# Kernel tuning notes

Hardware: AMD Instinct MI355X
Metric: run time of the kernel (lower is better)

Reference implementation:

```python
import jax, jax.numpy as jnp
import numpy as np
from jax import lax

N, L, D = 8, 2048, 512
KS = [3, 5]
DECAY = 0.2


def setup_inputs() -> dict:
    key = jax.random.key(0)
    k1, k2, k3, k4, k5 = jax.random.split(key, 5)
    return {
        "qa_embed_data": jax.random.normal(k1, (N, L, D), dtype=jnp.float32),
        "conv_w3": jax.random.normal(k2, (D, 1, KS[0]), dtype=jnp.float32) * (1.0 / KS[0]),
        "conv_w5": jax.random.normal(k3, (D, 1, KS[1]), dtype=jnp.float32) * (1.0 / KS[1]),
        "fusion_w": jax.random.normal(k4, (D, 2 * D), dtype=jnp.float32) * 0.02,
        "fusion_b": jax.random.normal(k5, (D,), dtype=jnp.float32) * 0.02,
    }


def causal_depthwise_conv(x, w, k):
    # x: [N, L, C], w: [C, 1, k] (depthwise, groups=C). Left-pad by k-1 (causal).
    xc = jnp.transpose(x, (0, 2, 1))  # [N, C, L]
    y = lax.conv_general_dilated(
        xc, w, window_strides=(1,), padding=[(k - 1, 0)],
        feature_group_count=x.shape[-1],
        dimension_numbers=("NCH", "OIH", "NCH"))
    return jnp.transpose(y, (0, 2, 1))  # [N, L, C]


def squash(v):
    norm = jnp.linalg.norm(v, axis=-1, keepdims=True)
    scale = norm ** 2 / (1.0 + norm ** 2)
    return scale * v / (norm + 1e-9)


def dynamic_routing(u, num_iterations):
    # u: [N, L, M, C]
    n, l, m, _ = u.shape
    logits = jnp.zeros((n, l, m), dtype=u.dtype)
    v = None
    for i in range(num_iterations):
        c = jax.nn.softmax(logits, axis=-1)
        s = jnp.einsum("nlm,nlmc->nlc", c, u)
        v = squash(s)
        if i < num_iterations - 1:
            logits = logits + jnp.einsum("nlmc,nlc->nlm", u, v)
    return v


def time_attention(x):
    # x: [N, L, C]; causal attention with exp(-decay*dist) bias -> add -decay*dist in log space
    l = x.shape[1]
    sim = jnp.einsum("nlc,nmc->nlm", x, x)  # [N, L, L]
    idx = jnp.arange(l)
    dist = (idx[:, None] - idx[None, :]).astype(x.dtype)  # query - key
    mask = dist >= 0  # lower-triangular causal mask
    ws = jnp.where(mask[None], sim - DECAY * dist[None], -jnp.inf)
    attn = jax.nn.softmax(ws, axis=-1)
    return jnp.einsum("nlm,nmc->nlc", attn, x)


def reference(qa_embed_data, conv_w3, conv_w5, fusion_w, fusion_b):
    trend3 = causal_depthwise_conv(qa_embed_data, conv_w3, KS[0])
    trend5 = causal_depthwise_conv(qa_embed_data, conv_w5, KS[1])
    seasonal = jnp.stack([qa_embed_data - trend3, qa_embed_data - trend5], axis=2)  # [N,L,2,C]
    trend = jnp.stack([trend3, trend5], axis=2)  # [N,L,2,C]
    seasonal_f = time_attention(dynamic_routing(seasonal, 3))
    trend_f = time_attention(dynamic_routing(trend, 3))
    cat = jnp.concatenate([seasonal_f, trend_f], axis=-1)  # [N,L,2C]
    return cat @ fusion_w.T + fusion_b
```

## Files before the change

### kernel.cpp

```cpp
#include <hip/hip_runtime.h>


typedef short     bf16x8 __attribute__((ext_vector_type(8)));
typedef float     f32x4  __attribute__((ext_vector_type(4)));
typedef unsigned short u16;
typedef u16       u16x8  __attribute__((ext_vector_type(8)));

#define NBATCH 8
#define LSEQ   2048
#define DCH    512
#define DPAD   520
#define DECAYF 0.2f
#define WTILES 4

typedef const __attribute__((address_space(1))) unsigned char* gas_t;
typedef __attribute__((address_space(3))) unsigned char* las_t;
__device__ __forceinline__ void dma16(const void* g, void* l) {
    __builtin_amdgcn_global_load_lds((gas_t)g, (las_t)l, 16, 0, 0);
}

__device__ __forceinline__ u16 f2bf(float f) {
    unsigned int u = __float_as_uint(f);
    u += 0x7fffu + ((u >> 16) & 1u);
    return (u16)(u >> 16);
}

__device__ __forceinline__ void wave_sum6(float& a, float& b, float& c,
                                          float& d, float& e, float& f) {
#pragma unroll
    for (int m = 1; m < 64; m <<= 1) {
        float ta = __shfl_xor(a, m, 64);
        float tb = __shfl_xor(b, m, 64);
        float tc = __shfl_xor(c, m, 64);
        float td = __shfl_xor(d, m, 64);
        float te = __shfl_xor(e, m, 64);
        float tf = __shfl_xor(f, m, 64);
        a += ta; b += tb; c += tc; d += td; e += te; f += tf;
    }
}

__global__ __launch_bounds__(256) void conv_route(
    const float* __restrict__ x, const float* __restrict__ w3, const float* __restrict__ w5,
    u16* __restrict__ vs, u16* __restrict__ vt)
{
    const int wid  = threadIdx.x >> 6;
    const int lane = threadIdx.x & 63;
    const int p = blockIdx.x * 4 + wid;
    const int n = p >> 11, l = p & (LSEQ - 1);
    const int c0 = lane * 8;

    float xm[5][8];
#pragma unroll
    for (int j = 0; j < 5; ++j) {
        int ll = l - j;
        if (ll >= 0) {
            const float4* sp = (const float4*)(x + ((size_t)(n*LSEQ + ll))*DCH + c0);
            float4 a = sp[0], b = sp[1];
            xm[j][0]=a.x; xm[j][1]=a.y; xm[j][2]=a.z; xm[j][3]=a.w;
            xm[j][4]=b.x; xm[j][5]=b.y; xm[j][6]=b.z; xm[j][7]=b.w;
        } else {
#pragma unroll
            for (int i = 0; i < 8; ++i) xm[j][i] = 0.f;
        }
    }
    float f3[24], f5[40];
#pragma unroll
    for (int k = 0; k < 6; ++k)  ((float4*)f3)[k] = ((const float4*)(w3 + (size_t)c0*3))[k];
#pragma unroll
    for (int k = 0; k < 10; ++k) ((float4*)f5)[k] = ((const float4*)(w5 + (size_t)c0*5))[k];

    float t3[8], t5[8], a0[8], a1[8];
#pragma unroll
    for (int i = 0; i < 8; ++i) {
        t3[i] = f3[i*3+0]*xm[2][i] + f3[i*3+1]*xm[1][i] + f3[i*3+2]*xm[0][i];
        t5[i] = f5[i*5+0]*xm[4][i] + f5[i*5+1]*xm[3][i] + f5[i*5+2]*xm[2][i]
              + f5[i*5+3]*xm[1][i] + f5[i*5+4]*xm[0][i];
        a0[i] = xm[0][i] - t3[i];
        a1[i] = xm[0][i] - t5[i];
    }

    float A1=0.f, B1=0.f, C1=0.f, A2=0.f, B2=0.f, C2=0.f;
#pragma unroll
    for (int i = 0; i < 8; ++i) {
        A1 += a0[i]*a0[i]; B1 += a0[i]*a1[i]; C1 += a1[i]*a1[i];
        A2 += t3[i]*t3[i]; B2 += t3[i]*t5[i]; C2 += t5[i]*t5[i];
    }
    wave_sum6(A1, B1, C1, A2, B2, C2);

    float ba0=0.f, ba1=0.f, bb0=0.f, bb1=0.f;
    float ca0=0.5f, ca1=0.5f, sca=0.f, cb0=0.5f, cb1=0.5f, scb=0.f;
#pragma unroll
    for (int it = 0; it < 3; ++it) {
        float mxa = fmaxf(ba0, ba1), mxb = fmaxf(bb0, bb1);
        float ea0 = __expf(ba0-mxa), ea1 = __expf(ba1-mxa);
        float eb0 = __expf(bb0-mxb), eb1 = __expf(bb1-mxb);
        float ia = 1.f/(ea0+ea1), ib = 1.f/(eb0+eb1);
        ca0 = ea0*ia; ca1 = ea1*ia; cb0 = eb0*ib; cb1 = eb1*ib;
        float na = ca0*ca0*A1 + 2.f*ca0*ca1*B1 + ca1*ca1*C1;
        float nb = cb0*cb0*A2 + 2.f*cb0*cb1*B2 + cb1*cb1*C2;
        sca = na / ((1.f + na) * (sqrtf(na) + 1e-9f));
        scb = nb / ((1.f + nb) * (sqrtf(nb) + 1e-9f));
        if (it < 2) {
            ba0 += sca*(ca0*A1 + ca1*B1);
            ba1 += sca*(ca0*B1 + ca1*C1);
            bb0 += scb*(cb0*A2 + cb1*B2);
            bb1 += scb*(cb0*B2 + cb1*C2);
        }
    }
    u16x8 pa, pb;
#pragma unroll
    for (int i = 0; i < 8; ++i) {
        pa[i] = f2bf(sca*(ca0*a0[i] + ca1*a1[i]));
        pb[i] = f2bf(scb*(cb0*t3[i] + cb1*t5[i]));
    }
    *(u16x8*)(vs + (size_t)p*DPAD + c0) = pa;
    *(u16x8*)(vt + (size_t)p*DPAD + c0) = pb;
}

__global__ __launch_bounds__(256) void transpose_vtile(
    const u16* __restrict__ vs, const u16* __restrict__ vt,
    u16* __restrict__ vsTt, u16* __restrict__ vtTt)
{
    __shared__ u16 T[64][65];
    const int z = blockIdx.z;
    const u16* src = ((z & 8) ? vt : vs) + (size_t)(z & 7) * LSEQ * DPAD;
    u16*       dst = ((z & 8) ? vtTt : vsTt) + (size_t)(z & 7) * 64 * DCH * 32;
    const int l0 = blockIdx.y * 64, c0 = blockIdx.x * 64;
    const int tid = threadIdx.x;
    const int rl = tid >> 3, cc = (tid & 7) * 8;
#pragma unroll
    for (int i = 0; i < 2; ++i) {
        int row = rl + i*32;
        *(u16x8*)(&T[row][cc]) = *(const u16x8*)(src + (size_t)(l0+row)*DPAD + c0 + cc);
    }
    __syncthreads();
    const int ch = tid >> 3;
    const int q3 = tid & 7;
    const int tt = q3 >> 2;
    const int sc = (q3 & 3) * 8;
#pragma unroll
    for (int i = 0; i < 2; ++i) {
        int c = ch + i*32;
        u16x8 o;
#pragma unroll
        for (int j = 0; j < 8; ++j) {
            int s = sc + j;
            int key = (s >> 1) + ((s & 1) << 4);
            o[j] = T[tt*32 + key][c];
        }
        *(u16x8*)(dst + (size_t)(blockIdx.y*2 + tt) * (DCH*32)
                      + (size_t)(c0 + c) * 32 + sc) = o;
    }
}

__global__ __launch_bounds__(256) void attn(
    const u16* __restrict__ vs, const u16* __restrict__ vt,
    const u16* __restrict__ vsTt, const u16* __restrict__ vtTt,
    u16* __restrict__ cat)
{
    __shared__ u16 Ks[33792/2];
    __shared__ u16 Vs[DCH*32];
    __shared__ unsigned int Ps32[4][16][20];

    const int inst = blockIdx.y;
    const int t = inst >> 3, n = inst & 7;
    const u16* src  = (t ? vt : vs) + (size_t)n * LSEQ * DPAD;
    const u16* srcT = (t ? vtTt : vsTt) + (size_t)n * 64 * DCH * 32;

    const int bx = blockIdx.x;
    const int r0 = (((bx & 7) << 2) | (bx >> 3)) * 64;

    const int tid  = threadIdx.x;
    const int wid  = tid >> 6, lane = tid & 63;
    const int l16  = lane & 15, quad = lane >> 4;

    bf16x8 qf[16];
    {
        const u16* qp = src + (size_t)(r0 + wid*16 + l16) * DPAD + quad*8;
#pragma unroll
        for (int kc = 0; kc < 16; ++kc) qf[kc] = *(const bf16x8*)(qp + kc*32);
    }

    f32x4 O[32];
#pragma unroll
    for (int i = 0; i < 32; ++i) O[i] = (f32x4){0.f, 0.f, 0.f, 0.f};
    f32x4 O2 = {0.f, 0.f, 0.f, 0.f};

    bf16x8 ones8;
#pragma unroll
    for (int i = 0; i < 8; ++i) ones8[i] = (short)0x3F80;

    const int kb_hi = (r0 >> 5) + 1;
    const int kb_lo = (kb_hi >= WTILES) ? kb_hi - (WTILES-1) : 0;

    {
        const u16* gK = src + (size_t)kb_lo * 32 * DPAD;
        for (int i = wid; i < 33; i += 4) dma16(gK + i*512 + lane*8, Ks + i*512);
    }

    for (int kb = kb_lo; kb <= kb_hi; ++kb) {
        __syncthreads();
        {
            const u16* gV = srcT + (size_t)kb * (DCH*32);
            for (int i = wid; i < 32; i += 4) dma16(gV + i*512 + lane*8, Vs + i*512);
        }

        f32x4 S0a = {0.f,0.f,0.f,0.f}, S1a = {0.f,0.f,0.f,0.f};
        f32x4 S0b = {0.f,0.f,0.f,0.f}, S1b = {0.f,0.f,0.f,0.f};
#pragma unroll
        for (int kc = 0; kc < 8; ++kc) {
            bf16x8 b0 = *(const bf16x8*)(Ks + (size_t)l16*DPAD + kc*32 + quad*8);
            bf16x8 b1 = *(const bf16x8*)(Ks + (size_t)(16+l16)*DPAD + kc*32 + quad*8);
            S0a = __builtin_amdgcn_mfma_f32_16x16x32_bf16(qf[kc], b0, S0a, 0, 0, 0);
            S1a = __builtin_amdgcn_mfma_f32_16x16x32_bf16(qf[kc], b1, S1a, 0, 0, 0);
        }
#pragma unroll
        for (int kc = 8; kc < 16; ++kc) {
            bf16x8 b0 = *(const bf16x8*)(Ks + (size_t)l16*DPAD + kc*32 + quad*8);
            bf16x8 b1 = *(const bf16x8*)(Ks + (size_t)(16+l16)*DPAD + kc*32 + quad*8);
            S0b = __builtin_amdgcn_mfma_f32_16x16x32_bf16(qf[kc], b0, S0b, 0, 0, 0);
            S1b = __builtin_amdgcn_mfma_f32_16x16x32_bf16(qf[kc], b1, S1b, 0, 0, 0);
        }
        f32x4 S0 = S0a + S0b, S1 = S1a + S1b;

        const int rowg = r0 + wid*16 + quad*4;
#pragma unroll
        for (int r = 0; r < 4; ++r) {
            int row = rowg + r;
            int d0  = row - (kb*32 + l16);
            int d1  = d0 - 16;
            float p0 = (d0 >= 0) ? __expf(fmaf(-DECAYF, (float)d0, S0[r] - 1.f)) : 0.f;
            float p1 = (d1 >= 0) ? __expf(fmaf(-DECAYF, (float)d1, S1[r] - 1.f)) : 0.f;
            Ps32[wid][quad*4 + r][l16] = ((unsigned)f2bf(p1) << 16) | (unsigned)f2bf(p0);
        }

        __syncthreads();
        if (kb < kb_hi) {
            const u16* gK = src + (size_t)(kb+1) * 32 * DPAD;
            for (int i = wid; i < 33; i += 4) dma16(gK + i*512 + lane*8, Ks + i*512);
        }

        bf16x8 pf = *(const bf16x8*)(&Ps32[wid][l16][quad*4]);
#pragma unroll
        for (int ct = 0; ct < 32; ++ct) {
            bf16x8 vf = *(const bf16x8*)(Vs + (size_t)(ct*16 + l16)*32 + quad*8);
            O[ct] = __builtin_amdgcn_mfma_f32_16x16x32_bf16(pf, vf, O[ct], 0, 0, 0);
        }
        O2 = __builtin_amdgcn_mfma_f32_16x16x32_bf16(pf, ones8, O2, 0, 0, 0);
    }

    float inv[4];
#pragma unroll
    for (int r = 0; r < 4; ++r) inv[r] = 1.f / O2[r];
    const size_t rowbase = (size_t)n * LSEQ + r0 + wid*16 + quad*4;
    const int colbase = t * 512 + l16;
#pragma unroll
    for (int ct = 0; ct < 32; ++ct) {
#pragma unroll
        for (int r = 0; r < 4; ++r)
            cat[(rowbase + r) * 1024 + colbase + ct*16] = f2bf(O[ct][r] * inv[r]);
    }
}

__global__ __launch_bounds__(256) void fusion_gemm(
    const u16* __restrict__ A, const float* __restrict__ W,
    const float* __restrict__ bias, float* __restrict__ out)
{
    __shared__ u16 As[128][72];
    __shared__ u16 Bs[128][72];
    const int m0 = blockIdx.x * 128;
    const int n0 = blockIdx.y * 128;
    const int tid = threadIdx.x;
    const int wid = tid >> 6, lane = tid & 63;
    const int l16 = lane & 15, quad = lane >> 4;
    const int wm = (wid >> 1) * 64, wn = (wid & 1) * 64;

    f32x4 acc[4][4];
#pragma unroll
    for (int i = 0; i < 4; ++i)
#pragma unroll
        for (int j = 0; j < 4; ++j) acc[i][j] = (f32x4){0.f, 0.f, 0.f, 0.f};

    for (int kb = 0; kb < 16; ++kb) {
#pragma unroll
        for (int i = 0; i < 4; ++i) {
            int id = tid + i*256;
            int row = id >> 3, kc = id & 7;
            *(u16x8*)(&As[row][kc*8]) = *(const u16x8*)(A + (size_t)(m0+row)*1024 + kb*64 + kc*8);
            const float4* wp = (const float4*)(W + (size_t)(n0+row)*1024 + kb*64 + kc*8);
            float4 wa = wp[0], wb4 = wp[1];
            u16x8 bb;
            bb[0]=f2bf(wa.x); bb[1]=f2bf(wa.y); bb[2]=f2bf(wa.z); bb[3]=f2bf(wa.w);
            bb[4]=f2bf(wb4.x); bb[5]=f2bf(wb4.y); bb[6]=f2bf(wb4.z); bb[7]=f2bf(wb4.w);
            *(u16x8*)(&Bs[row][kc*8]) = bb;
        }
        __syncthreads();
#pragma unroll
        for (int k2 = 0; k2 < 2; ++k2) {
            bf16x8 af[4], bfr[4];
#pragma unroll
            for (int i = 0; i < 4; ++i) {
                af[i]  = *(const bf16x8*)(&As[wm + i*16 + l16][k2*32 + quad*8]);
                bfr[i] = *(const bf16x8*)(&Bs[wn + i*16 + l16][k2*32 + quad*8]);
            }
#pragma unroll
            for (int i = 0; i < 4; ++i)
#pragma unroll
                for (int j = 0; j < 4; ++j)
                    acc[i][j] = __builtin_amdgcn_mfma_f32_16x16x32_bf16(af[i], bfr[j], acc[i][j], 0, 0, 0);
        }
        __syncthreads();
    }
#pragma unroll
    for (int j = 0; j < 4; ++j) {
        int col = n0 + wn + j*16 + l16;
        float bv = bias[col];
#pragma unroll
        for (int i = 0; i < 4; ++i) {
            int rowb = m0 + wm + i*16 + quad*4;
#pragma unroll
            for (int r = 0; r < 4; ++r)
                out[(size_t)(rowb + r)*512 + col] = acc[i][j][r] + bv;
        }
    }
}

extern "C" void kernel_launch(void* const* d_in, const int* in_sizes, int n_in,
                              void* d_out, int out_size, void* d_ws, size_t ws_size,
                              hipStream_t stream)
{
    (void)in_sizes; (void)n_in; (void)out_size; (void)ws_size;
    const float* x  = (const float*)d_in[0];
    const float* w3 = (const float*)d_in[1];
    const float* w5 = (const float*)d_in[2];
    const float* fw = (const float*)d_in[3];
    const float* fb = (const float*)d_in[4];
    float* out = (float*)d_out;

    const size_t SZP = (size_t)NBATCH * LSEQ * DPAD;
    const size_t SZT = (size_t)NBATCH * 64 * DCH * 32;
    u16* vs   = (u16*)d_ws;
    u16* vt   = vs   + SZP;
    u16* vsTt = vt   + SZP;
    u16* vtTt = vsTt + SZT;
    u16* cat  = vtTt + SZT;

    conv_route    <<<4096, 256, 0, stream>>>(x, w3, w5, vs, vt);
    transpose_vtile<<<dim3(8, 32, 16), 256, 0, stream>>>(vs, vt, vsTt, vtTt);
    attn          <<<dim3(32, 16), 256, 0, stream>>>(vs, vt, vsTt, vtTt, cat);
    fusion_gemm   <<<dim3(128, 4), 256, 0, stream>>>(cat, fw, fb, out);
}
```

Measured before the change: 193.1 us.

## Fuse transpose into conv_route, pre-cast fusion weights, retile fusion GEMM with LDS DMA

The separate transpose kernel is folded into conv_route. Each 512-thread block now computes 32 consecutive positions, with each wave handling 4 of them while keeping a sliding register window of x rows, and writes the transposed tiles from shared memory. The fusion GEMM weight is cast to bf16 once in a small kernel. The GEMM then uses 64x128 tiles loaded by global_load_lds DMA into XOR-swizzled LDS. This removes a kernel launch and a global round trip for the transpose, plus the repeated per-block fp32-to-bf16 weight conversion. The cost is an extra cast kernel and fewer waves per position in conv_route.

```diff
diff --git a/kernel.cpp b/kernel.cpp
--- a/kernel.cpp
+++ b/kernel.cpp
@@ -5,11 +5,13 @@
 typedef float     f32x4  __attribute__((ext_vector_type(4)));
 typedef unsigned short u16;
 typedef u16       u16x8  __attribute__((ext_vector_type(8)));
+typedef u16       u16x4  __attribute__((ext_vector_type(4)));
 
 #define NBATCH 8
 #define LSEQ   2048
 #define DCH    512
 #define DPAD   520
+#define TPAD   524
 #define DECAYF 0.2f
 #define WTILES 4
 
@@ -39,20 +41,30 @@
     }
 }
 
-__global__ __launch_bounds__(256) void conv_route(
+__global__ __launch_bounds__(512) void conv_route(
     const float* __restrict__ x, const float* __restrict__ w3, const float* __restrict__ w5,
-    u16* __restrict__ vs, u16* __restrict__ vt)
-{
-    const int wid  = threadIdx.x >> 6;
-    const int lane = threadIdx.x & 63;
-    const int p = blockIdx.x * 4 + wid;
-    const int n = p >> 11, l = p & (LSEQ - 1);
-    const int c0 = lane * 8;
+    u16* __restrict__ vs, u16* __restrict__ vt,
+    u16* __restrict__ vsTt, u16* __restrict__ vtTt)
+{
+    __shared__ u16 Ts[2][32][TPAD];
+
+    const int tid  = threadIdx.x;
+    const int wid  = tid >> 6, lane = tid & 63;
+    const int pb   = blockIdx.x * 32 + wid * 4;
+    const int n    = pb >> 11;
+    const int l0   = pb & (LSEQ - 1);
+    const int c0   = lane * 8;
+
+    float f3[24], f5[40];
+#pragma unroll
+    for (int k = 0; k < 6; ++k)  ((float4*)f3)[k] = ((const float4*)(w3 + (size_t)c0*3))[k];
+#pragma unroll
+    for (int k = 0; k < 10; ++k) ((float4*)f5)[k] = ((const float4*)(w5 + (size_t)c0*5))[k];
 
     float xm[5][8];
 #pragma unroll
     for (int j = 0; j < 5; ++j) {
-        int ll = l - j;
+        int ll = l0 - j;
         if (ll >= 0) {
             const float4* sp = (const float4*)(x + ((size_t)(n*LSEQ + ll))*DCH + c0);
             float4 a = sp[0], b = sp[1];
@@ -63,93 +75,86 @@
             for (int i = 0; i < 8; ++i) xm[j][i] = 0.f;
         }
     }
-    float f3[24], f5[40];
-#pragma unroll
-    for (int k = 0; k < 6; ++k)  ((float4*)f3)[k] = ((const float4*)(w3 + (size_t)c0*3))[k];
-#pragma unroll
-    for (int k = 0; k < 10; ++k) ((float4*)f5)[k] = ((const float4*)(w5 + (size_t)c0*5))[k];
-
-    float t3[8], t5[8], a0[8], a1[8];
-#pragma unroll
-    for (int i = 0; i < 8; ++i) {
-        t3[i] = f3[i*3+0]*xm[2][i] + f3[i*3+1]*xm[1][i] + f3[i*3+2]*xm[0][i];
-        t5[i] = f5[i*5+0]*xm[4][i] + f5[i*5+1]*xm[3][i] + f5[i*5+2]*xm[2][i]
-              + f5[i*5+3]*xm[1][i] + f5[i*5+4]*xm[0][i];
-        a0[i] = xm[0][i] - t3[i];
-        a1[i] = xm[0][i] - t5[i];
-    }
-
-    float A1=0.f, B1=0.f, C1=0.f, A2=0.f, B2=0.f, C2=0.f;
-#pragma unroll
-    for (int i = 0; i < 8; ++i) {
-        A1 += a0[i]*a0[i]; B1 += a0[i]*a1[i]; C1 += a1[i]*a1[i];
-        A2 += t3[i]*t3[i]; B2 += t3[i]*t5[i]; C2 += t5[i]*t5[i];
-    }
-    wave_sum6(A1, B1, C1, A2, B2, C2);
-
-    float ba0=0.f, ba1=0.f, bb0=0.f, bb1=0.f;
-    float ca0=0.5f, ca1=0.5f, sca=0.f, cb0=0.5f, cb1=0.5f, scb=0.f;
-#pragma unroll
-    for (int it = 0; it < 3; ++it) {
-        float mxa = fmaxf(ba0, ba1), mxb = fmaxf(bb0, bb1);
-        float ea0 = __expf(ba0-mxa), ea1 = __expf(ba1-mxa);
-        float eb0 = __expf(bb0-mxb), eb1 = __expf(bb1-mxb);
-        float ia = 1.f/(ea0+ea1), ib = 1.f/(eb0+eb1);
-        ca0 = ea0*ia; ca1 = ea1*ia; cb0 = eb0*ib; cb1 = eb1*ib;
-        float na = ca0*ca0*A1 + 2.f*ca0*ca1*B1 + ca1*ca1*C1;
-        float nb = cb0*cb0*A2 + 2.f*cb0*cb1*B2 + cb1*cb1*C2;
-        sca = na / ((1.f + na) * (sqrtf(na) + 1e-9f));
-        scb = nb / ((1.f + nb) * (sqrtf(nb) + 1e-9f));
-        if (it < 2) {
-            ba0 += sca*(ca0*A1 + ca1*B1);
-            ba1 += sca*(ca0*B1 + ca1*C1);
-            bb0 += scb*(cb0*A2 + cb1*B2);
-            bb1 += scb*(cb0*B2 + cb1*C2);
-        }
-    }
-    u16x8 pa, pb;
-#pragma unroll
-    for (int i = 0; i < 8; ++i) {
-        pa[i] = f2bf(sca*(ca0*a0[i] + ca1*a1[i]));
-        pb[i] = f2bf(scb*(cb0*t3[i] + cb1*t5[i]));
-    }
-    *(u16x8*)(vs + (size_t)p*DPAD + c0) = pa;
-    *(u16x8*)(vt + (size_t)p*DPAD + c0) = pb;
-}
-
-__global__ __launch_bounds__(256) void transpose_vtile(
-    const u16* __restrict__ vs, const u16* __restrict__ vt,
-    u16* __restrict__ vsTt, u16* __restrict__ vtTt)
-{
-    __shared__ u16 T[64][65];
-    const int z = blockIdx.z;
-    const u16* src = ((z & 8) ? vt : vs) + (size_t)(z & 7) * LSEQ * DPAD;
-    u16*       dst = ((z & 8) ? vtTt : vsTt) + (size_t)(z & 7) * 64 * DCH * 32;
-    const int l0 = blockIdx.y * 64, c0 = blockIdx.x * 64;
-    const int tid = threadIdx.x;
-    const int rl = tid >> 3, cc = (tid & 7) * 8;
-#pragma unroll
-    for (int i = 0; i < 2; ++i) {
-        int row = rl + i*32;
-        *(u16x8*)(&T[row][cc]) = *(const u16x8*)(src + (size_t)(l0+row)*DPAD + c0 + cc);
+
+#pragma unroll
+    for (int s = 0; s < 4; ++s) {
+        const int l = l0 + s;
+        if (s > 0) {
+#pragma unroll
+            for (int j = 4; j > 0; --j)
+#pragma unroll
+                for (int i = 0; i < 8; ++i) xm[j][i] = xm[j-1][i];
+            const float4* sp = (const float4*)(x + ((size_t)(n*LSEQ + l))*DCH + c0);
+            float4 a = sp[0], b = sp[1];
+            xm[0][0]=a.x; xm[0][1]=a.y; xm[0][2]=a.z; xm[0][3]=a.w;
+            xm[0][4]=b.x; xm[0][5]=b.y; xm[0][6]=b.z; xm[0][7]=b.w;
+        }
+
+        float t3[8], t5[8], a0[8], a1[8];
+#pragma unroll
+        for (int i = 0; i < 8; ++i) {
+            t3[i] = f3[i*3+0]*xm[2][i] + f3[i*3+1]*xm[1][i] + f3[i*3+2]*xm[0][i];
+            t5[i] = f5[i*5+0]*xm[4][i] + f5[i*5+1]*xm[3][i] + f5[i*5+2]*xm[2][i]
+                  + f5[i*5+3]*xm[1][i] + f5[i*5+4]*xm[0][i];
+            a0[i] = xm[0][i] - t3[i];
+            a1[i] = xm[0][i] - t5[i];
+        }
+
+        float A1=0.f, B1=0.f, C1=0.f, A2=0.f, B2=0.f, C2=0.f;
+#pragma unroll
+        for (int i = 0; i < 8; ++i) {
+            A1 += a0[i]*a0[i]; B1 += a0[i]*a1[i]; C1 += a1[i]*a1[i];
+            A2 += t3[i]*t3[i]; B2 += t3[i]*t5[i]; C2 += t5[i]*t5[i];
+        }
+        wave_sum6(A1, B1, C1, A2, B2, C2);
+
+        float ba0=0.f, ba1=0.f, bb0=0.f, bb1=0.f;
+        float ca0=0.5f, ca1=0.5f, sca=0.f, cb0=0.5f, cb1=0.5f, scb=0.f;
+#pragma unroll
+        for (int it = 0; it < 3; ++it) {
+            float mxa = fmaxf(ba0, ba1), mxb = fmaxf(bb0, bb1);
+            float ea0 = __expf(ba0-mxa), ea1 = __expf(ba1-mxa);
+            float eb0 = __expf(bb0-mxb), eb1 = __expf(bb1-mxb);
+            float ia = 1.f/(ea0+ea1), ib = 1.f/(eb0+eb1);
+            ca0 = ea0*ia; ca1 = ea1*ia; cb0 = eb0*ib; cb1 = eb1*ib;
+            float na = ca0*ca0*A1 + 2.f*ca0*ca1*B1 + ca1*ca1*C1;
+            float nb = cb0*cb0*A2 + 2.f*cb0*cb1*B2 + cb1*cb1*C2;
+            sca = na / ((1.f + na) * (sqrtf(na) + 1e-9f));
+            scb = nb / ((1.f + nb) * (sqrtf(nb) + 1e-9f));
+            if (it < 2) {
+                ba0 += sca*(ca0*A1 + ca1*B1);
+                ba1 += sca*(ca0*B1 + ca1*C1);
+                bb0 += scb*(cb0*A2 + cb1*B2);
+                bb1 += scb*(cb0*B2 + cb1*C2);
+            }
+        }
+
+        u16x8 pa, pb8;
+#pragma unroll
+        for (int i = 0; i < 8; ++i) {
+            pa[i]  = f2bf(sca*(ca0*a0[i] + ca1*a1[i]));
+            pb8[i] = f2bf(scb*(cb0*t3[i] + cb1*t5[i]));
+        }
+        *(u16x8*)(vs + (size_t)(pb + s)*DPAD + c0) = pa;
+        *(u16x8*)(vt + (size_t)(pb + s)*DPAD + c0) = pb8;
+        *(u16x8*)(&Ts[0][wid*4 + s][c0]) = pa;
+        *(u16x8*)(&Ts[1][wid*4 + s][c0]) = pb8;
     }
     __syncthreads();
-    const int ch = tid >> 3;
-    const int q3 = tid & 7;
-    const int tt = q3 >> 2;
-    const int sc = (q3 & 3) * 8;
-#pragma unroll
-    for (int i = 0; i < 2; ++i) {
-        int c = ch + i*32;
+
+#pragma unroll
+    for (int k = 0; k < 8; ++k) {
+        int id = k*512 + tid;
+        int z = id >> 11, rem = id & 2047, ch = rem >> 2, so = rem & 3;
         u16x8 o;
 #pragma unroll
         for (int j = 0; j < 8; ++j) {
-            int s = sc + j;
+            int s = so*8 + j;
             int key = (s >> 1) + ((s & 1) << 4);
-            o[j] = T[tt*32 + key][c];
-        }
-        *(u16x8*)(dst + (size_t)(blockIdx.y*2 + tt) * (DCH*32)
-                      + (size_t)(c0 + c) * 32 + sc) = o;
+            o[j] = Ts[z][key][ch];
+        }
+        u16* dst = (z ? vtTt : vsTt) + (size_t)blockIdx.x * (DCH*32);
+        *(u16x8*)(dst + ch*32 + so*8) = o;
     }
 }
 
@@ -262,62 +267,76 @@
     }
 }
 
+__global__ __launch_bounds__(256) void cast_w(const float* __restrict__ w, u16* __restrict__ wb)
+{
+    int id = blockIdx.x * 256 + threadIdx.x;
+    float4 f = ((const float4*)w)[id];
+    u16x4 o;
+    o[0] = f2bf(f.x); o[1] = f2bf(f.y); o[2] = f2bf(f.z); o[3] = f2bf(f.w);
+    ((u16x4*)wb)[id] = o;
+}
+
 __global__ __launch_bounds__(256) void fusion_gemm(
-    const u16* __restrict__ A, const float* __restrict__ W,
+    const u16* __restrict__ A, const u16* __restrict__ Wb,
     const float* __restrict__ bias, float* __restrict__ out)
 {
-    __shared__ u16 As[128][72];
-    __shared__ u16 Bs[128][72];
-    const int m0 = blockIdx.x * 128;
+    __shared__ u16 As[64*64];
+    __shared__ u16 Bs[128*64];
+    const int m0 = blockIdx.x * 64;
     const int n0 = blockIdx.y * 128;
     const int tid = threadIdx.x;
     const int wid = tid >> 6, lane = tid & 63;
     const int l16 = lane & 15, quad = lane >> 4;
-    const int wm = (wid >> 1) * 64, wn = (wid & 1) * 64;
-
-    f32x4 acc[4][4];
+
+    f32x4 acc[4][2];
 #pragma unroll
     for (int i = 0; i < 4; ++i)
 #pragma unroll
-        for (int j = 0; j < 4; ++j) acc[i][j] = (f32x4){0.f, 0.f, 0.f, 0.f};
+        for (int j = 0; j < 2; ++j) acc[i][j] = (f32x4){0.f, 0.f, 0.f, 0.f};
 
     for (int kb = 0; kb < 16; ++kb) {
+        __syncthreads();
+#pragma unroll
+        for (int i = 0; i < 2; ++i) {
+            int q = i*256 + tid, r = q >> 3, kp = q & 7;
+            int kl = kp ^ (r & 7);
+            dma16(A + (size_t)(m0 + r)*1024 + kb*64 + kl*8, As + q*8);
+        }
 #pragma unroll
         for (int i = 0; i < 4; ++i) {
-            int id = tid + i*256;
-            int row = id >> 3, kc = id & 7;
-            *(u16x8*)(&As[row][kc*8]) = *(const u16x8*)(A + (size_t)(m0+row)*1024 + kb*64 + kc*8);
-            const float4* wp = (const float4*)(W + (size_t)(n0+row)*1024 + kb*64 + kc*8);
-            float4 wa = wp[0], wb4 = wp[1];
-            u16x8 bb;
-            bb[0]=f2bf(wa.x); bb[1]=f2bf(wa.y); bb[2]=f2bf(wa.z); bb[3]=f2bf(wa.w);
-            bb[4]=f2bf(wb4.x); bb[5]=f2bf(wb4.y); bb[6]=f2bf(wb4.z); bb[7]=f2bf(wb4.w);
-            *(u16x8*)(&Bs[row][kc*8]) = bb;
+            int q = i*256 + tid, r = q >> 3, kp = q & 7;
+            int kl = kp ^ (r & 7);
+            dma16(Wb + (size_t)(n0 + r)*1024 + kb*64 + kl*8, Bs + q*8);
         }
         __syncthreads();
 #pragma unroll
         for (int k2 = 0; k2 < 2; ++k2) {
-            bf16x8 af[4], bfr[4];
+            const int kl = k2*4 + quad;
+            bf16x8 af[4], bf2[2];
 #pragma unroll
             for (int i = 0; i < 4; ++i) {
-                af[i]  = *(const bf16x8*)(&As[wm + i*16 + l16][k2*32 + quad*8]);
-                bfr[i] = *(const bf16x8*)(&Bs[wn + i*16 + l16][k2*32 + quad*8]);
+                int r = i*16 + l16;
+                af[i] = *(const bf16x8*)(As + r*64 + (kl ^ (r & 7))*8);
             }
 #pragma unroll
+            for (int j = 0; j < 2; ++j) {
+                int r = wid*32 + j*16 + l16;
+                bf2[j] = *(const bf16x8*)(Bs + r*64 + (kl ^ (r & 7))*8);
+            }
+#pragma unroll
             for (int i = 0; i < 4; ++i)
 #pragma unroll
-                for (int j = 0; j < 4; ++j)
-                    acc[i][j] = __builtin_amdgcn_mfma_f32_16x16x32_bf16(af[i], bfr[j], acc[i][j], 0, 0, 0);
-        }
-        __syncthreads();
-    }
-#pragma unroll
-    for (int j = 0; j < 4; ++j) {
-        int col = n0 + wn + j*16 + l16;
+                for (int j = 0; j < 2; ++j)
+                    acc[i][j] = __builtin_amdgcn_mfma_f32_16x16x32_bf16(af[i], bf2[j], acc[i][j], 0, 0, 0);
+        }
+    }
+#pragma unroll
+    for (int j = 0; j < 2; ++j) {
+        int col = n0 + wid*32 + j*16 + l16;
         float bv = bias[col];
 #pragma unroll
         for (int i = 0; i < 4; ++i) {
-            int rowb = m0 + wm + i*16 + quad*4;
+            int rowb = m0 + i*16 + quad*4;
 #pragma unroll
             for (int r = 0; r < 4; ++r)
                 out[(size_t)(rowb + r)*512 + col] = acc[i][j][r] + bv;
@@ -344,9 +363,10 @@
     u16* vsTt = vt   + SZP;
     u16* vtTt = vsTt + SZT;
     u16* cat  = vtTt + SZT;
-
-    conv_route    <<<4096, 256, 0, stream>>>(x, w3, w5, vs, vt);
-    transpose_vtile<<<dim3(8, 32, 16), 256, 0, stream>>>(vs, vt, vsTt, vtTt);
-    attn          <<<dim3(32, 16), 256, 0, stream>>>(vs, vt, vsTt, vtTt, cat);
-    fusion_gemm   <<<dim3(128, 4), 256, 0, stream>>>(cat, fw, fb, out);
-}
+    u16* wb   = cat  + (size_t)NBATCH*LSEQ*1024;
+
+    cast_w     <<<512, 256, 0, stream>>>(fw, wb);
+    conv_route <<<512, 512, 0, stream>>>(x, w3, w5, vs, vt, vsTt, vtTt);
+    attn       <<<dim3(32, 16), 256, 0, stream>>>(vs, vt, vsTt, vtTt, cat);
+    fusion_gemm<<<dim3(256, 4), 256, 0, stream>>>(cat, wb, fb, out);
+}
```

New measurement: 171.2 us. 1.13x faster.
